# Performance work log

Hardware: AMD Instinct MI355X
Metric: run time of the kernel (lower is better)

Reference implementation:

```python
import jax, jax.numpy as jnp
import numpy as np

DIM = 4096
NH = 32
NKV = 8
HD = DIM // NH          # 128
REP = NH // NKV          # 4
B = 1
T = 2048
THETA = 500000.0
NEG = -1e9


def setup_inputs() -> dict:
    key = jax.random.key(0)
    ks = jax.random.split(key, 6)
    x = jax.random.normal(ks[0], (B, T, DIM), jnp.float32)
    # RoPE tables (real/imag parts of freqs_cis = exp(i * t * inv_freq))
    inv_freq = 1.0 / (THETA ** (np.arange(0, HD, 2, dtype=np.float32) / HD))  # (HD/2,)
    ang = np.outer(np.arange(T, dtype=np.float32), inv_freq)                  # (T, HD/2)
    freqs_cos = jnp.asarray(np.cos(ang), jnp.float32)
    freqs_sin = jnp.asarray(np.sin(ang), jnp.float32)
    # additive causal mask for prefill (pos=0): (T, T)
    mask = jnp.where(np.tril(np.ones((T, T), dtype=bool)), 0.0, NEG).astype(jnp.float32)
    cache_k = jnp.zeros((B, T, NKV, HD), jnp.float32)
    cache_v = jnp.zeros((B, T, NKV, HD), jnp.float32)
    s = 0.02
    wk_w = jax.random.normal(ks[1], (NKV * HD, DIM), jnp.float32) * s
    wk_b = jnp.zeros((NKV * HD,), jnp.float32)
    wv_w = jax.random.normal(ks[2], (NKV * HD, DIM), jnp.float32) * s
    wv_b = jnp.zeros((NKV * HD,), jnp.float32)
    wo_w = jax.random.normal(ks[3], (DIM, DIM), jnp.float32) * s
    wo_b = jnp.zeros((DIM,), jnp.float32)
    return dict(x=x, freqs_cos=freqs_cos, freqs_sin=freqs_sin, mask=mask,
                cache_k=cache_k, cache_v=cache_v,
                wk_w=wk_w, wk_b=wk_b, wv_w=wv_w, wv_b=wv_b,
                wo_w=wo_w, wo_b=wo_b, pos=0)


def _rope(t, cos, sin):
    # t: (B, T, H, HD); pairs (even, odd) form complex numbers
    tr = t.reshape(*t.shape[:-1], HD // 2, 2)
    re, im = tr[..., 0], tr[..., 1]
    c = cos[None, :, None, :]
    s = sin[None, :, None, :]
    out = jnp.stack([re * c - im * s, re * s + im * c], axis=-1)
    return out.reshape(t.shape)


def reference(x, freqs_cos, freqs_sin, mask, cache_k, cache_v,
              wk_w, wk_b, wv_w, wv_b, wo_w, wo_b, pos):
    Bx, Tx, D = x.shape
    # NOTE: faithful to source bug -- q projection uses wo (shared with output proj)
    q = x @ wo_w.T + wo_b                        # (B, T, D)
    k = x @ wk_w.T + wk_b                        # (B, T, NKV*HD)
    v = x @ wv_w.T + wv_b
    q = q.reshape(Bx, Tx, NH, HD)
    k = k.reshape(Bx, Tx, NKV, HD)
    v = v.reshape(Bx, Tx, NKV, HD)
    q = _rope(q, freqs_cos, freqs_sin)
    k = _rope(k, freqs_cos, freqs_sin)
    # KV-cache append then read back [:pos+T]
    ck = cache_k.at[:Bx, pos:pos + Tx].set(k)
    cv = cache_v.at[:Bx, pos:pos + Tx].set(v)
    k = ck[:Bx, :pos + Tx]
    v = cv[:Bx, :pos + Tx]
    # repeat_kv (GQA expansion)
    k = jnp.repeat(k, REP, axis=2)               # (B, S, NH, HD)
    v = jnp.repeat(v, REP, axis=2)
    scale = 1.0 / jnp.sqrt(jnp.float32(HD))
    scores = jnp.einsum('bqhd,bkhd->bhqk', q, k) * scale
    scores = scores + mask[None, None, :, :]
    p = jax.nn.softmax(scores.astype(jnp.float32), axis=-1)
    out = jnp.einsum('bhqk,bkhd->bqhd', p, v).reshape(Bx, Tx, D)
    return out @ wo_w.T + wo_b
```

## Files before the change

### kernel.cpp

```cpp
#include <hip/hip_runtime.h>
#include <stdint.h>
#include <stddef.h>

#define T_SEQ 2048
#define DIM   4096
#define NH    32
#define NKV   8
#define HD    128
#define KVD   (NKV*HD)

typedef __attribute__((ext_vector_type(8))) short short8;
typedef __attribute__((ext_vector_type(4))) float floatx4;
typedef __attribute__((ext_vector_type(2))) unsigned int uintx2;

static __device__ __forceinline__ float bf2f(short u) {
    union { unsigned int i; float f; } c; c.i = ((unsigned int)(unsigned short)u) << 16; return c.f;
}
static __device__ __forceinline__ short f2bf(float f) {
    union { float f; unsigned int u; } c; c.f = f;
    unsigned int r = c.u + 0x7fff + ((c.u >> 16) & 1);
    return (short)(r >> 16);
}
static __device__ __forceinline__ short8 ld8_f2b(const float* p) {
    floatx4 a = *(const floatx4*)p;
    floatx4 b = *(const floatx4*)(p + 4);
    short8 r;
    r[0]=f2bf(a[0]); r[1]=f2bf(a[1]); r[2]=f2bf(a[2]); r[3]=f2bf(a[3]);
    r[4]=f2bf(b[0]); r[5]=f2bf(b[1]); r[6]=f2bf(b[2]); r[7]=f2bf(b[3]);
    return r;
}

#define GLD16(g, l) __builtin_amdgcn_global_load_lds( \
    (const __attribute__((address_space(1))) unsigned int*)(g), \
    (__attribute__((address_space(3))) unsigned int*)(l), 16, 0, 0)

__global__ __launch_bounds__(256)
void cvt_bf16(const float* __restrict__ x, const float* __restrict__ wk,
              const float* __restrict__ wv, const float* __restrict__ wo,
              short* __restrict__ xb, short* __restrict__ wkb,
              short* __restrict__ wvb, short* __restrict__ wob) {
    size_t i8 = ((size_t)blockIdx.x * 256 + threadIdx.x) * 8;
    const float* src; short* dst; size_t off;
    if (i8 < 8388608)        { src = x;  dst = xb;  off = i8; }
    else if (i8 < 12582912)  { src = wk; dst = wkb; off = i8 - 8388608; }
    else if (i8 < 16777216)  { src = wv; dst = wvb; off = i8 - 12582912; }
    else                     { src = wo; dst = wob; off = i8 - 16777216; }
    *(short8*)(dst + off) = ld8_f2b(src + off);
}

template<bool C_F32>
static __device__ __forceinline__
void gemm_core(const short* __restrict__ A, const short* __restrict__ B,
               const float* __restrict__ bias, void* __restrict__ Cp,
               int N, int K, int bm, int bn) {
    __shared__ short sA0[128*32];
    __shared__ short sA1[128*32];
    __shared__ short sA2[128*32];
    __shared__ short sB0[128*32];
    __shared__ short sB1[128*32];
    __shared__ short sB2[128*32];
    const int tid  = threadIdx.x;
    const int wave = tid >> 6, lane = tid & 63;
    const int l15  = lane & 15, lq = lane >> 4;
    const int wm   = (wave >> 1) * 64, wn = (wave & 1) * 64;

    floatx4 acc[4][4];
    #pragma unroll
    for (int i = 0; i < 4; i++)
        #pragma unroll
        for (int j = 0; j < 4; j++)
            acc[i][j] = (floatx4)(0.0f);

    const int c0 = tid, c1 = 256 + tid;
    const int r0 = c0 >> 2, k0 = (c0 & 3) * 8;
    const int r1 = c1 >> 2, k1 = (c1 & 3) * 8;
    const short* pA0 = A + (size_t)(bm + r0) * K + k0;
    const short* pA1 = A + (size_t)(bm + r1) * K + k1;
    const short* pB0 = B + (size_t)(bn + r0) * K + k0;
    const short* pB1 = B + (size_t)(bn + r1) * K + k1;

    auto stage = [&](short* dA, short* dB, int kt) {
        GLD16(pA0 + kt, dA + c0 * 8);
        GLD16(pA1 + kt, dA + c1 * 8);
        GLD16(pB0 + kt, dB + c0 * 8);
        GLD16(pB1 + kt, dB + c1 * 8);
    };
    auto compute = [&](const short* dA, const short* dB) {
        short8 af[4], bfr[4];
        #pragma unroll
        for (int mi = 0; mi < 4; mi++)
            af[mi] = *(const short8*)&dA[(wm + mi*16 + l15)*32 + lq*8];
        #pragma unroll
        for (int ni = 0; ni < 4; ni++)
            bfr[ni] = *(const short8*)&dB[(wn + ni*16 + l15)*32 + lq*8];
        #pragma unroll
        for (int mi = 0; mi < 4; mi++)
            #pragma unroll
            for (int ni = 0; ni < 4; ni++)
                acc[mi][ni] = __builtin_amdgcn_mfma_f32_16x16x32_bf16(af[mi], bfr[ni], acc[mi][ni], 0, 0, 0);
    };

    stage(sA0, sB0, 0);
    stage(sA1, sB1, 32);
    short *cA = sA0, *cB = sB0;
    short *nA = sA1, *nB = sB1;
    short *fA = sA2, *fB = sB2;

    const int nt = K >> 5;
    for (int t = 0; t < nt - 1; ++t) {
        asm volatile("s_waitcnt vmcnt(4)" ::: "memory");
        __builtin_amdgcn_s_barrier();
        if (t + 2 < nt) stage(fA, fB, (t + 2) * 32);
        compute(cA, cB);
        short* x;
        x = cA; cA = nA; nA = fA; fA = x;
        x = cB; cB = nB; nB = fB; fB = x;
    }
    asm volatile("s_waitcnt vmcnt(0)" ::: "memory");
    __builtin_amdgcn_s_barrier();
    compute(cA, cB);

    #pragma unroll
    for (int ni = 0; ni < 4; ni++) {
        int col = bn + wn + ni*16 + l15;
        float bv = bias[col];
        #pragma unroll
        for (int mi = 0; mi < 4; mi++) {
            int row = bm + wm + mi*16 + lq*4;
            #pragma unroll
            for (int r = 0; r < 4; r++) {
                float v = acc[mi][ni][r] + bv;
                if (C_F32) ((float*)Cp)[(size_t)(row + r)*N + col] = v;
                else       ((short*)Cp)[(size_t)(row + r)*N + col] = f2bf(v);
            }
        }
    }
}

template<bool C_F32>
__global__ __launch_bounds__(256)
void gemm_bt(const short* __restrict__ A, const short* __restrict__ B,
             const float* __restrict__ bias, void* __restrict__ Cp,
             int N, int K) {
    gemm_core<C_F32>(A, B, bias, Cp, N, K, blockIdx.y * 128, blockIdx.x * 128);
}

__global__ __launch_bounds__(256)
void gemm_qkv(const short* __restrict__ A,
              const short* __restrict__ Bq, const float* __restrict__ bq, short* __restrict__ Cq,
              const short* __restrict__ Bk, const float* __restrict__ bk, short* __restrict__ Ck,
              const short* __restrict__ Bv, const float* __restrict__ bv, short* __restrict__ Cv) {
    const int ct = blockIdx.x;
    const short* B; const float* bias; short* C; int N, bn;
    if (ct < 32)      { B = Bq; bias = bq; C = Cq; N = DIM; bn = ct*128; }
    else if (ct < 40) { B = Bk; bias = bk; C = Ck; N = KVD; bn = (ct-32)*128; }
    else              { B = Bv; bias = bv; C = Cv; N = KVD; bn = (ct-40)*128; }
    gemm_core<false>(A, B, bias, C, N, DIM, blockIdx.y * 128, bn);
}

#define QSC (0.08838834764831845f * 1.4426950408889634f)

__global__ __launch_bounds__(256)
void rope_k(short* __restrict__ Q, short* __restrict__ Kc,
            const float* __restrict__ fc, const float* __restrict__ fs) {
    int idx = blockIdx.x * 256 + threadIdx.x;
    const int NQ = T_SEQ * NH  * (HD/2);
    const int NK = T_SEQ * NKV * (HD/2);
    short* base; int t, i; size_t off; float sc;
    if (idx < NQ) {
        i = idx & 63;
        int th = idx >> 6;
        t = th >> 5;
        off = (size_t)th * HD + i*2;
        base = Q; sc = QSC;
    } else if (idx < NQ + NK) {
        int kidx = idx - NQ;
        i = kidx & 63;
        int th = kidx >> 6;
        t = th >> 3;
        off = (size_t)th * HD + i*2;
        base = Kc; sc = 1.0f;
    } else return;
    float re = bf2f(base[off]), im = bf2f(base[off+1]);
    float c = fc[t*64 + i], s = fs[t*64 + i];
    base[off]   = f2bf((re*c - im*s)*sc);
    base[off+1] = f2bf((re*s + im*c)*sc);
}

__global__ __launch_bounds__(256)
void vtrans(const short* __restrict__ V, short* __restrict__ Vt) {
    __shared__ short sT[64*72];
    const int tid = threadIdx.x;
    const int bt = blockIdx.x, bd = blockIdx.y;
    #pragma unroll
    for (int i = 0; i < 2; i++) {
        int c = i*256 + tid;
        int r = c >> 3, c8 = (c & 7) * 8;
        *(short8*)&sT[r*72 + c8] = *(const short8*)(V + (size_t)(bt*64 + r)*KVD + bd*64 + c8);
    }
    __syncthreads();
    #pragma unroll
    for (int i = 0; i < 2; i++) {
        int c = i*256 + tid;
        int d = c >> 3, t8 = (c & 7) * 8;
        short8 o;
        #pragma unroll
        for (int j = 0; j < 8; j++) o[j] = sT[(t8 + j)*72 + d];
        *(short8*)(Vt + (size_t)(bd*64 + d)*T_SEQ + bt*64 + t8) = o;
    }
}

__global__ __launch_bounds__(256, 2)
void flash_attn(const short* __restrict__ Q, const short* __restrict__ Kc,
                const short* __restrict__ Vt, short* __restrict__ O) {
    __shared__ short sK0[64*128];
    __shared__ short sK1[64*128];
    __shared__ short sV0[128*64];
    __shared__ short sV1[128*64];
    __shared__ short sP[4*2048];
    const int tid  = threadIdx.x;
    const int wave = tid >> 6, lane = tid & 63;
    const int l15  = lane & 15, lq = lane >> 4;
    const int sw   = l15 & 7;
    const int kvg  = blockIdx.y;
    const int qt   = (blockIdx.y < 4) ? (int)blockIdx.x : 63 - (int)blockIdx.x;
    const int hl   = wave;
    const int qb   = qt * 32;

    short8 qf[2][4];
    #pragma unroll
    for (int mi = 0; mi < 2; mi++)
        #pragma unroll
        for (int ks = 0; ks < 4; ks++)
            qf[mi][ks] = *(const short8*)(Q + (size_t)(qb + mi*16 + l15)*DIM
                                          + kvg*512 + hl*128 + ks*32 + lq*8);

    char* pw = (char*)(sP + wave*2048);

    int kc_r[4], kc_jg[4], vc_r[4], vc_jg[4];
    #pragma unroll
    for (int i = 0; i < 4; i++) {
        int c = i*256 + tid;
        kc_r[i]  = c >> 4;
        kc_jg[i] = (c & 15) ^ (kc_r[i] & 7);
        vc_r[i]  = c >> 3;
        vc_jg[i] = (c & 7) ^ (vc_r[i] & 7);
    }
    auto stage = [&](short* dK, short* dV, int kt) {
        #pragma unroll
        for (int i = 0; i < 4; i++) {
            int c = i*256 + tid;
            GLD16(Kc + (size_t)(kt*64 + kc_r[i])*KVD + kvg*HD + kc_jg[i]*8,
                  dK + c*8);
            GLD16(Vt + (size_t)(kvg*HD + vc_r[i])*T_SEQ + kt*64 + vc_jg[i]*8,
                  dV + c*8);
        }
    };

    float m_r[2] = {-1e30f, -1e30f};
    float l_r[2] = {0.0f, 0.0f};
    floatx4 o_acc[2][8];
    #pragma unroll
    for (int mi = 0; mi < 2; mi++)
        #pragma unroll
        for (int nd = 0; nd < 8; nd++) o_acc[mi][nd] = (floatx4)(0.0f);

    const int ktmax = qt >> 1;
    stage(sK0, sV0, 0);
    __syncthreads();

    for (int kt = 0; kt <= ktmax; kt++) {
        short* bK = (kt & 1) ? sK1 : sK0;
        short* bV = (kt & 1) ? sV1 : sV0;
        if (kt < ktmax) stage((kt & 1) ? sK0 : sK1, (kt & 1) ? sV0 : sV1, kt + 1);

        floatx4 s_acc[2][4];
        #pragma unroll
        for (int mi = 0; mi < 2; mi++)
            #pragma unroll
            for (int ni = 0; ni < 4; ni++) s_acc[mi][ni] = (floatx4)(0.0f);
        __builtin_amdgcn_s_setprio(1);
        #pragma unroll
        for (int ks = 0; ks < 4; ks++)
            #pragma unroll
            for (int ni = 0; ni < 4; ni++) {
                short8 kf = *(const short8*)&bK[(ni*16 + l15)*128
                                                + (((ks*4 + lq) ^ sw)*8)];
                s_acc[0][ni] = __builtin_amdgcn_mfma_f32_16x16x32_bf16(kf, qf[0][ks], s_acc[0][ni], 0, 0, 0);
                s_acc[1][ni] = __builtin_amdgcn_mfma_f32_16x16x32_bf16(kf, qf[1][ks], s_acc[1][ni], 0, 0, 0);
            }
        __builtin_amdgcn_s_setprio(0);

        const bool last = (kt == ktmax);

        #pragma unroll
        for (int mi = 0; mi < 2; mi++) {
            float sv[4][4];
            float mx = -1e30f;
            const int qrow = qb + mi*16 + l15;
            #pragma unroll
            for (int ni = 0; ni < 4; ni++)
                #pragma unroll
                for (int r = 0; r < 4; r++) {
                    float x = s_acc[mi][ni][r];
                    if (last) {
                        int kcol = kt*64 + ni*16 + lq*4 + r;
                        x = (kcol <= qrow) ? x : -1e30f;
                    }
                    sv[ni][r] = x;
                    mx = fmaxf(mx, x);
                }
            mx = fmaxf(mx, __shfl_xor(mx, 16));
            mx = fmaxf(mx, __shfl_xor(mx, 32));

            if (__any(mx - m_r[mi] > 8.0f)) {
                float mn = fmaxf(m_r[mi], mx);
                float a  = __builtin_amdgcn_exp2f(m_r[mi] - mn);
                m_r[mi] = mn;
                l_r[mi] *= a;
                float ar[4];
                #pragma unroll
                for (int r = 0; r < 4; r++) ar[r] = __shfl(a, lq*4 + r);
                #pragma unroll
                for (int nd = 0; nd < 8; nd++)
                    #pragma unroll
                    for (int r = 0; r < 4; r++) o_acc[mi][nd][r] *= ar[r];
            }

            float rs = 0.0f;
            #pragma unroll
            for (int ni = 0; ni < 4; ni++)
                #pragma unroll
                for (int r = 0; r < 4; r++) {
                    float p = __builtin_amdgcn_exp2f(sv[ni][r] - m_r[mi]);
                    sv[ni][r] = p;
                    rs += p;
                }
            rs += __shfl_xor(rs, 16);
            rs += __shfl_xor(rs, 32);
            l_r[mi] += rs;

            char* rowp = pw + (mi*16 + l15)*128 + (lq & 1)*8;
            #pragma unroll
            for (int ni = 0; ni < 4; ni++) {
                unsigned int lo, hi;
                asm("v_cvt_pk_bf16_f32 %0, %1, %2" : "=v"(lo) : "v"(sv[ni][0]), "v"(sv[ni][1]));
                asm("v_cvt_pk_bf16_f32 %0, %1, %2" : "=v"(hi) : "v"(sv[ni][2]), "v"(sv[ni][3]));
                int kc = ni*2 + (lq >> 1);
                *(uintx2*)(rowp + ((kc ^ sw) * 16)) = (uintx2){lo, hi};
            }
        }

        __builtin_amdgcn_s_setprio(1);
        #pragma unroll
        for (int ks = 0; ks < 2; ks++) {
            short8 pf[2];
            #pragma unroll
            for (int mi = 0; mi < 2; mi++)
                pf[mi] = *(const short8*)(pw + (mi*16 + l15)*128
                                          + (((ks*4 + lq) ^ sw)*16));
            #pragma unroll
            for (int nd = 0; nd < 8; nd++) {
                short8 vf = *(const short8*)&bV[(nd*16 + l15)*64
                                                + (((ks*4 + lq) ^ sw)*8)];
                o_acc[0][nd] = __builtin_amdgcn_mfma_f32_16x16x32_bf16(pf[0], vf, o_acc[0][nd], 0, 0, 0);
                o_acc[1][nd] = __builtin_amdgcn_mfma_f32_16x16x32_bf16(pf[1], vf, o_acc[1][nd], 0, 0, 0);
            }
        }
        __builtin_amdgcn_s_setprio(0);

        __syncthreads();
    }

    float rec[2][4];
    #pragma unroll
    for (int mi = 0; mi < 2; mi++) {
        float rv = 1.0f / l_r[mi];
        #pragma unroll
        for (int r = 0; r < 4; r++) rec[mi][r] = __shfl(rv, lq*4 + r);
    }
    #pragma unroll
    for (int mi = 0; mi < 2; mi++)
        #pragma unroll
        for (int nd = 0; nd < 8; nd++) {
            int col = (kvg*4 + hl)*HD + nd*16 + l15;
            #pragma unroll
            for (int r = 0; r < 4; r++) {
                int row = qb + mi*16 + lq*4 + r;
                O[(size_t)row*DIM + col] = f2bf(o_acc[mi][nd][r] * rec[mi][r]);
            }
        }
}

extern "C" void kernel_launch(void* const* d_in, const int* in_sizes, int n_in,
                              void* d_out, int out_size, void* d_ws, size_t ws_size,
                              hipStream_t stream) {
    const float* x    = (const float*)d_in[0];
    const float* fc   = (const float*)d_in[1];
    const float* fs   = (const float*)d_in[2];
    const float* wk_w = (const float*)d_in[6];
    const float* wk_b = (const float*)d_in[7];
    const float* wv_w = (const float*)d_in[8];
    const float* wv_b = (const float*)d_in[9];
    const float* wo_w = (const float*)d_in[10];
    const float* wo_b = (const float*)d_in[11];
    float* out = (float*)d_out;

    short* xb  = (short*)d_ws;
    short* wkb = xb  + 8388608;
    short* wvb = wkb + 4194304;
    short* wob = wvb + 4194304;
    short* Q   = wob + 16777216;
    short* K   = Q   + 8388608;
    short* V   = K   + 2097152;
    short* Vt  = V   + 2097152;
    short* AO  = Vt  + 2097152;

    cvt_bf16<<<dim3(16384), dim3(256), 0, stream>>>(x, wk_w, wv_w, wo_w, xb, wkb, wvb, wob);

    gemm_qkv<<<dim3(48, 16), dim3(256), 0, stream>>>(
        xb, wob, wo_b, Q, wkb, wk_b, K, wvb, wv_b, V);

    int nrope = T_SEQ*NH*(HD/2) + T_SEQ*NKV*(HD/2);
    rope_k<<<dim3((nrope + 255)/256), dim3(256), 0, stream>>>(Q, K, fc, fs);

    vtrans<<<dim3(32, 16), dim3(256), 0, stream>>>(V, Vt);

    flash_attn<<<dim3(64, 8), dim3(256), 0, stream>>>(Q, K, Vt, AO);

    gemm_bt<true><<<dim3(32, 16), dim3(256), 0, stream>>>(AO, wob, wo_b, out, DIM, DIM);
}
```

Baseline: 487.3 us.

## Use 512-thread 128x256 ping-pong GEMM for Q and output projections

Adds a new GEMM kernel with 8 waves, 128x256 tiles, a K-step of 64, double-buffered LDS loads issued directly from global memory, XOR-swizzled LDS layout, and MFMA phases split around the next-stage prefetch with raised wave priority. The Q projection and the output projection now use this kernel, while the K/V projections move to a separate smaller launch using the old core. The aim is more operand reuse per tile and better overlap of loads with MFMA work. In exchange, the fused QKV launch becomes two launches, and the 256-block grid may underfill the GPU's compute units.

```diff
diff --git a/kernel.cpp b/kernel.cpp
--- a/kernel.cpp
+++ b/kernel.cpp
@@ -46,6 +46,127 @@
     else if (i8 < 16777216)  { src = wv; dst = wvb; off = i8 - 12582912; }
     else                     { src = wo; dst = wob; off = i8 - 16777216; }
     *(short8*)(dst + off) = ld8_f2b(src + off);
+}
+
+template<bool C_F32>
+__global__ __launch_bounds__(512, 1)
+void gemm8p(const short* __restrict__ A, const short* __restrict__ B,
+            const float* __restrict__ bias, void* __restrict__ Cp,
+            int N, int K) {
+    __shared__ short sA[2][128*64];
+    __shared__ short sB[2][256*64];
+    const int tid  = threadIdx.x;
+    const int wave = tid >> 6, lane = tid & 63;
+    const int l15  = lane & 15, lq = lane >> 4;
+    const int sw   = l15 & 7;
+    const int wm   = (wave >> 2) * 64;
+    const int wn   = (wave & 3) * 64;
+    const int bm   = blockIdx.y * 128, bn = blockIdx.x * 256;
+
+    floatx4 acc[4][4];
+    #pragma unroll
+    for (int i = 0; i < 4; i++)
+        #pragma unroll
+        for (int j = 0; j < 4; j++)
+            acc[i][j] = (floatx4)(0.0f);
+
+    const short* pa[2]; int ca[2];
+    #pragma unroll
+    for (int i = 0; i < 2; i++) {
+        int c = i*512 + tid, row = c >> 3, jg = (c & 7) ^ (row & 7);
+        pa[i] = A + (size_t)(bm + row) * K + jg*8;
+        ca[i] = c;
+    }
+    const short* pb[4]; int cb[4];
+    #pragma unroll
+    for (int i = 0; i < 4; i++) {
+        int c = i*512 + tid, row = c >> 3, jg = (c & 7) ^ (row & 7);
+        pb[i] = B + (size_t)(bn + row) * K + jg*8;
+        cb[i] = c;
+    }
+    auto stage = [&](int buf, int kt) {
+        #pragma unroll
+        for (int i = 0; i < 2; i++) GLD16(pa[i] + kt, &sA[buf][ca[i]*8]);
+        #pragma unroll
+        for (int i = 0; i < 4; i++) GLD16(pb[i] + kt, &sB[buf][cb[i]*8]);
+    };
+
+    stage(0, 0);
+    stage(1, 64);
+
+    const int nt = K >> 6;
+    int buf = 0;
+    for (int t = 0; t < nt; ++t) {
+        if (t < nt - 1) asm volatile("s_waitcnt vmcnt(6)" ::: "memory");
+        else            asm volatile("s_waitcnt vmcnt(0)" ::: "memory");
+        __builtin_amdgcn_s_barrier();
+
+        const short* lA = sA[buf];
+        const short* lB = sB[buf];
+        short8 af[4][2], bf[4][2];
+        #pragma unroll
+        for (int mi = 0; mi < 4; mi++)
+            #pragma unroll
+            for (int ks = 0; ks < 2; ks++)
+                af[mi][ks] = *(const short8*)&lA[(wm + mi*16 + l15)*64
+                                                 + (((ks*4 + lq) ^ sw)*8)];
+        #pragma unroll
+        for (int ni = 0; ni < 2; ni++)
+            #pragma unroll
+            for (int ks = 0; ks < 2; ks++)
+                bf[ni][ks] = *(const short8*)&lB[(wn + ni*16 + l15)*64
+                                                 + (((ks*4 + lq) ^ sw)*8)];
+        asm volatile("s_waitcnt lgkmcnt(0)" ::: "memory");
+        __builtin_amdgcn_sched_barrier(0);
+        __builtin_amdgcn_s_setprio(1);
+        #pragma unroll
+        for (int ks = 0; ks < 2; ks++)
+            #pragma unroll
+            for (int mi = 0; mi < 4; mi++)
+                #pragma unroll
+                for (int ni = 0; ni < 2; ni++)
+                    acc[mi][ni] = __builtin_amdgcn_mfma_f32_16x16x32_bf16(
+                        af[mi][ks], bf[ni][ks], acc[mi][ni], 0, 0, 0);
+        __builtin_amdgcn_s_setprio(0);
+
+        #pragma unroll
+        for (int ni = 2; ni < 4; ni++)
+            #pragma unroll
+            for (int ks = 0; ks < 2; ks++)
+                bf[ni][ks] = *(const short8*)&lB[(wn + ni*16 + l15)*64
+                                                 + (((ks*4 + lq) ^ sw)*8)];
+        asm volatile("s_waitcnt lgkmcnt(0)" ::: "memory");
+        __builtin_amdgcn_sched_barrier(0);
+        __builtin_amdgcn_s_barrier();
+        if (t + 2 < nt) stage(buf, (t + 2) << 6);
+        __builtin_amdgcn_s_setprio(1);
+        #pragma unroll
+        for (int ks = 0; ks < 2; ks++)
+            #pragma unroll
+            for (int mi = 0; mi < 4; mi++)
+                #pragma unroll
+                for (int ni = 2; ni < 4; ni++)
+                    acc[mi][ni] = __builtin_amdgcn_mfma_f32_16x16x32_bf16(
+                        af[mi][ks], bf[ni][ks], acc[mi][ni], 0, 0, 0);
+        __builtin_amdgcn_s_setprio(0);
+        buf ^= 1;
+    }
+
+    #pragma unroll
+    for (int ni = 0; ni < 4; ni++) {
+        int col = bn + wn + ni*16 + l15;
+        float bv = bias[col];
+        #pragma unroll
+        for (int mi = 0; mi < 4; mi++) {
+            int row = bm + wm + mi*16 + lq*4;
+            #pragma unroll
+            for (int r = 0; r < 4; r++) {
+                float v = acc[mi][ni][r] + bv;
+                if (C_F32) ((float*)Cp)[(size_t)(row + r)*N + col] = v;
+                else       ((short*)Cp)[(size_t)(row + r)*N + col] = f2bf(v);
+            }
+        }
+    }
 }
 
 template<bool C_F32>
@@ -137,25 +258,14 @@
     }
 }
 
-template<bool C_F32>
 __global__ __launch_bounds__(256)
-void gemm_bt(const short* __restrict__ A, const short* __restrict__ B,
-             const float* __restrict__ bias, void* __restrict__ Cp,
-             int N, int K) {
-    gemm_core<C_F32>(A, B, bias, Cp, N, K, blockIdx.y * 128, blockIdx.x * 128);
-}
-
-__global__ __launch_bounds__(256)
-void gemm_qkv(const short* __restrict__ A,
-              const short* __restrict__ Bq, const float* __restrict__ bq, short* __restrict__ Cq,
-              const short* __restrict__ Bk, const float* __restrict__ bk, short* __restrict__ Ck,
-              const short* __restrict__ Bv, const float* __restrict__ bv, short* __restrict__ Cv) {
-    const int ct = blockIdx.x;
-    const short* B; const float* bias; short* C; int N, bn;
-    if (ct < 32)      { B = Bq; bias = bq; C = Cq; N = DIM; bn = ct*128; }
-    else if (ct < 40) { B = Bk; bias = bk; C = Ck; N = KVD; bn = (ct-32)*128; }
-    else              { B = Bv; bias = bv; C = Cv; N = KVD; bn = (ct-40)*128; }
-    gemm_core<false>(A, B, bias, C, N, DIM, blockIdx.y * 128, bn);
+void gemm_kv(const short* __restrict__ A,
+             const short* __restrict__ Bk, const float* __restrict__ bk, short* __restrict__ Ck,
+             const short* __restrict__ Bv, const float* __restrict__ bv, short* __restrict__ Cv) {
+    const short* B = blockIdx.z ? Bv : Bk;
+    const float* bias = blockIdx.z ? bv : bk;
+    short* C = blockIdx.z ? Cv : Ck;
+    gemm_core<false>(A, B, bias, C, KVD, DIM, blockIdx.y * 128, blockIdx.x * 128);
 }
 
 #define QSC (0.08838834764831845f * 1.4426950408889634f)
@@ -418,8 +528,8 @@
 
     cvt_bf16<<<dim3(16384), dim3(256), 0, stream>>>(x, wk_w, wv_w, wo_w, xb, wkb, wvb, wob);
 
-    gemm_qkv<<<dim3(48, 16), dim3(256), 0, stream>>>(
-        xb, wob, wo_b, Q, wkb, wk_b, K, wvb, wv_b, V);
+    gemm8p<false><<<dim3(16, 16), dim3(512), 0, stream>>>(xb, wob, wo_b, Q, DIM, DIM);
+    gemm_kv<<<dim3(8, 16, 2), dim3(256), 0, stream>>>(xb, wkb, wk_b, K, wvb, wv_b, V);
 
     int nrope = T_SEQ*NH*(HD/2) + T_SEQ*NKV*(HD/2);
     rope_k<<<dim3((nrope + 255)/256), dim3(256), 0, stream>>>(Q, K, fc, fs);
@@ -428,5 +538,5 @@
 
     flash_attn<<<dim3(64, 8), dim3(256), 0, stream>>>(Q, K, Vt, AO);
 
-    gemm_bt<true><<<dim3(32, 16), dim3(256), 0, stream>>>(AO, wob, wo_b, out, DIM, DIM);
-}
+    gemm8p<true><<<dim3(16, 16), dim3(512), 0, stream>>>(AO, wob, wo_b, out, DIM, DIM);
+}
```

New measurement: 482.7 us. Within noise of the previous version (-1.0%).
